# Kernel tuning notes

Measured on AMD Instinct MI355X. Metric: run time of the kernel, lower is better.

## Reference

```python
import jax, jax.numpy as jnp
import numpy as np

EMB_DIM = 32
UID_TGT = 200000
IID_TGT = 50000
BATCH = 128
TOPK = 50000          # hardcoded inside test_source_free branch
TARGET_LABEL = 4.0    # module-level target rating constant


def setup_inputs() -> dict:
    key = jax.random.key(0)
    k1, k2, k3, k4, k5 = jax.random.split(key, 5)
    # x: column 0 = item id (stored as float, like the torch code), cols 1: = src_rate_pre
    iid = jax.random.randint(k1, (BATCH,), 0, IID_TGT).astype(jnp.float32)
    src_rate = jax.random.normal(k2, (BATCH, EMB_DIM), dtype=jnp.float32)
    x = jnp.concatenate([iid[:, None], src_rate], axis=1)  # [B, 1+D]
    uid_weight = 0.1 * jax.random.normal(k3, (UID_TGT, EMB_DIM), dtype=jnp.float32)
    iid_weight = 0.1 * jax.random.normal(k4, (IID_TGT, EMB_DIM), dtype=jnp.float32)
    rp_weight = 0.1 * jax.random.normal(k5, (EMB_DIM, EMB_DIM), dtype=jnp.float32)
    return {"x": x, "uid_weight": uid_weight, "iid_weight": iid_weight, "rp_weight": rp_weight}


def reference(x, uid_weight, iid_weight, rp_weight):
    # === stage == 'test_source_free' ===
    iid = x[:, 0].astype(jnp.int32)                     # [B]
    iid_emb = iid_weight[iid]                           # [B, D] item embedding gather
    src_rate_pre = x[:, 1:] @ rp_weight.T               # [B, D] Linear(emb,emb,bias=False)
    # |uid_emb . src_rate - target|  (torch: [U,B]; here kept [B,U])
    predict_rate = jnp.abs(src_rate_pre @ uid_weight.T - TARGET_LABEL)  # [B, U]
    # torch: full sort ascending + take first TOPK  ==  bottom-TOPK per row
    _, topk_idx = jax.lax.top_k(-predict_rate, TOPK)    # [B, TOPK]
    # voted rating = <selected user emb, item emb>; compute all dots once,
    # then gather (same math as gathering [B,TOPK,D] embeddings and dotting).
    all_scores = iid_emb @ uid_weight.T                 # [B, U]
    voted_rating = jnp.take_along_axis(all_scores, topk_idx, axis=1)  # [B, TOPK]
    mean_rating = jnp.mean(voted_rating, axis=1)        # [B]
    return mean_rating
```

## Files before the change

### kernel.cpp

```cpp
#include <hip/hip_runtime.h>
#include <hip/hip_bf16.h>
#include <stdint.h>

#define EMB    32
#define BATCH  128
#define NU     200000
#define KSEL   50000
#define XCOLS  33
#define TILE   64
#define SLOTS  64

#define OFF_SPRE   0
#define OFF_IIDE   16384
#define OFF_GHIST  32768
#define OFF_BASE16 163840
#define OFF_PREFIX 164352
#define OFF_M2     164864
#define OFF_EQ     165376
#define OFF_CAND   173568

__global__ void prep_kernel(const float* __restrict__ x,
                            const float* __restrict__ iid_w,
                            const float* __restrict__ rp,
                            const float* __restrict__ uid,
                            float* __restrict__ s_pre,
                            float* __restrict__ iid_emb,
                            uint32_t* __restrict__ base16) {
    const int b = blockIdx.x;
    const int t = threadIdx.x;
    __shared__ float xr[EMB];
    if (t < EMB) xr[t] = x[b * XCOLS + 1 + t];
    __syncthreads();
    if (t < EMB) {
        float acc = 0.f;
        #pragma unroll
        for (int k = 0; k < EMB; ++k) acc += xr[k] * rp[t * EMB + k];
        s_pre[b * EMB + t] = acc;
    } else {
        const int d = t - EMB;
        const int iid = (int)x[b * XCOLS];
        iid_emb[b * EMB + d] = iid_w[(size_t)iid * EMB + d];
    }
    __syncthreads();
    if (t == 0) {
        float dot = 0.f;
        #pragma unroll
        for (int k = 0; k < EMB; ++k) dot += s_pre[b * EMB + k] * uid[k];
        const uint32_t bits = __float_as_uint(fabsf(dot - 4.0f));
        const uint32_t hi = bits >> 16;
        base16[b] = (hi > 128u) ? (hi - 128u) : 0u;
    }
}

__global__ void zero_kernel(uint32_t* __restrict__ p, int n) {
    int i = blockIdx.x * blockDim.x + threadIdx.x;
    if (i < n) p[i] = 0u;
}

__global__ __launch_bounds__(1024)
void sweep1_kernel(const float* __restrict__ s_pre,
                   const float* __restrict__ uid,
                   const uint32_t* __restrict__ base16,
                   uint32_t* __restrict__ ghist,
                   int jchunk) {
    extern __shared__ uint32_t smem1[];
    uint32_t* hist = smem1;
    float* tiles = (float*)(smem1 + 128 * 257);
    const int t  = threadIdx.x;
    const int b  = t & 127;
    const int jl = t >> 7;
    for (int i = t; i < 128 * 257; i += 1024) hist[i] = 0u;
    float s[EMB];
    #pragma unroll
    for (int d = 0; d < EMB; ++d) s[d] = s_pre[b * EMB + d];
    const uint32_t base = base16[b];

    const int j0 = blockIdx.x * jchunk;
    const int jend = min(j0 + jchunk, NU);
    const int nt = (jend - j0 + TILE - 1) / TILE;
    const int srow = t >> 4;
    const int sq   = t & 15;

    {
        const int j = j0 + srow;
        float2 v = make_float2(0.f, 0.f);
        if (j < NU) v = *(const float2*)(uid + (size_t)j * EMB + sq * 2);
        *(float2*)(tiles + srow * EMB + sq * 2) = v;
    }
    __syncthreads();

    for (int tt = 0; tt < nt; ++tt) {
        const int jt = j0 + tt * TILE;
        const bool has_next = (tt + 1 < nt);
        float2 vnext = make_float2(0.f, 0.f);
        if (has_next) {
            const int j = jt + TILE + srow;
            if (j < NU) vnext = *(const float2*)(uid + (size_t)j * EMB + sq * 2);
        }
        const float* tp = tiles + (tt & 1) * (TILE * EMB);
        const int lim = min(TILE, jend - jt);
        for (int jj = jl; jj < lim; jj += 8) {
            const float4* u4 = (const float4*)(tp + jj * EMB);
            float dot = 0.f;
            #pragma unroll
            for (int q = 0; q < 8; ++q) {
                float4 u = u4[q];
                dot += s[4*q+0]*u.x + s[4*q+1]*u.y + s[4*q+2]*u.z + s[4*q+3]*u.w;
            }
            const uint32_t bits = __float_as_uint(fabsf(dot - 4.0f));
            int digit = (int)(bits >> 16) - (int)base;
            digit = digit < 0 ? 0 : (digit > 255 ? 255 : digit);
            atomicAdd(&hist[b * 257 + digit], 1u);
        }
        if (has_next) {
            *(float2*)(tiles + ((tt + 1) & 1) * (TILE * EMB) + srow * EMB + sq * 2) = vnext;
        }
        __syncthreads();
    }
    for (int i = t; i < 128 * 256; i += 1024) {
        const uint32_t c = hist[(i >> 8) * 257 + (i & 255)];
        if (c) atomicAdd(&ghist[i], c);
    }
}

__global__ void scan1_kernel(const uint32_t* __restrict__ ghist,
                             const uint32_t* __restrict__ base16,
                             uint32_t* __restrict__ prefix16,
                             uint32_t* __restrict__ m2) {
    const int b = threadIdx.x;
    uint32_t cum = 0, before = 0;
    int c1 = 255;
    for (int d = 0; d < 256; ++d) {
        const uint32_t c = ghist[b * 256 + d];
        if (cum + c >= (uint32_t)KSEL) { c1 = d; before = cum; break; }
        cum += c;
        if (d == 255) before = cum;
    }
    prefix16[b] = base16[b] + (uint32_t)c1;
    m2[b] = (uint32_t)KSEL - before;
}

__global__ __launch_bounds__(1024)
void sweep2_kernel(const float* __restrict__ s_pre,
                   const float* __restrict__ iid_emb,
                   const float* __restrict__ uid,
                   const uint32_t* __restrict__ prefix16,
                   uint32_t* __restrict__ eq_cnt,
                   float* __restrict__ sum_part,
                   uint64_t* __restrict__ cand,
                   int cap, int jchunk) {
    extern __shared__ char smem2[];
    uint64_t* lcand = (uint64_t*)smem2;
    float*    tiles = (float*)(smem2 + 65536);
    uint32_t* lcnt  = (uint32_t*)(smem2 + 65536 + 16384);
    uint32_t* lbase = (uint32_t*)(smem2 + 65536 + 16384 + 512);
    float*    sums  = (float*)(smem2 + 65536 + 16384 + 1024);
    const int t  = threadIdx.x;
    const int b  = t & 127;
    const int jl = t >> 7;
    if (t < 128) lcnt[t] = 0u;
    float s[EMB], e[EMB];
    #pragma unroll
    for (int d = 0; d < EMB; ++d) { s[d] = s_pre[b*EMB+d]; e[d] = iid_emb[b*EMB+d]; }
    const uint32_t pfx = prefix16[b];

    const int j0 = blockIdx.x * jchunk;
    const int jend = min(j0 + jchunk, NU);
    const int nt = (jend - j0 + TILE - 1) / TILE;
    const int srow = t >> 4;
    const int sq   = t & 15;

    {
        const int j = j0 + srow;
        float2 v = make_float2(0.f, 0.f);
        if (j < NU) v = *(const float2*)(uid + (size_t)j * EMB + sq * 2);
        *(float2*)(tiles + srow * EMB + sq * 2) = v;
    }
    __syncthreads();

    float local = 0.f;
    for (int tt = 0; tt < nt; ++tt) {
        const int jt = j0 + tt * TILE;
        const bool has_next = (tt + 1 < nt);
        float2 vnext = make_float2(0.f, 0.f);
        if (has_next) {
            const int j = jt + TILE + srow;
            if (j < NU) vnext = *(const float2*)(uid + (size_t)j * EMB + sq * 2);
        }
        const float* tp = tiles + (tt & 1) * (TILE * EMB);
        const int lim = min(TILE, jend - jt);
        for (int jj = jl; jj < lim; jj += 8) {
            const float4* u4 = (const float4*)(tp + jj * EMB);
            float dot = 0.f, dv = 0.f;
            #pragma unroll
            for (int q = 0; q < 8; ++q) {
                float4 u = u4[q];
                dot += s[4*q+0]*u.x + s[4*q+1]*u.y + s[4*q+2]*u.z + s[4*q+3]*u.w;
                dv  += e[4*q+0]*u.x + e[4*q+1]*u.y + e[4*q+2]*u.z + e[4*q+3]*u.w;
            }
            const uint32_t bits = __float_as_uint(fabsf(dot - 4.0f));
            const uint32_t hi = bits >> 16;
            if (hi < pfx) {
                local += dv;
            } else if (hi == pfx) {
                const uint32_t pos = atomicAdd(&lcnt[b], 1u);
                const uint64_t pk = ((uint64_t)bits << 32) | (uint32_t)(jt + jj);
                if (pos < (uint32_t)SLOTS) {
                    lcand[b * SLOTS + pos] = pk;
                } else {
                    const uint32_t g = atomicAdd(&eq_cnt[b * 16], 1u);
                    if (g < (uint32_t)cap) cand[(size_t)b * cap + g] = pk;
                }
            }
        }
        if (has_next) {
            *(float2*)(tiles + ((tt + 1) & 1) * (TILE * EMB) + srow * EMB + sq * 2) = vnext;
        }
        __syncthreads();
    }
    sums[t] = local;
    __syncthreads();
    if (t < 128) {
        float acc = 0.f;
        #pragma unroll
        for (int l = 0; l < 8; ++l) acc += sums[l * 128 + t];
        sum_part[blockIdx.x * 128 + t] = acc;
        const uint32_t n = min(lcnt[t], (uint32_t)SLOTS);
        lbase[t] = atomicAdd(&eq_cnt[t * 16], n);
    }
    __syncthreads();
    for (int i = t; i < 128 * SLOTS; i += 1024) {
        const int bb = i >> 6;
        const int sl = i & 63;
        if (sl < (int)min(lcnt[bb], (uint32_t)SLOTS)) {
            const uint32_t p = lbase[bb] + (uint32_t)sl;
            if (p < (uint32_t)cap) cand[(size_t)bb * cap + p] = lcand[i];
        }
    }
}

__global__ __launch_bounds__(256)
void final_kernel(const float* __restrict__ iid_emb,
                  const float* __restrict__ uid,
                  const uint32_t* __restrict__ m2_,
                  const uint32_t* __restrict__ eq_cnt,
                  const float* __restrict__ sum_part,
                  const uint64_t* __restrict__ cand,
                  int cap, float* __restrict__ out) {
    const int b = blockIdx.x;
    const int t = threadIdx.x;
    __shared__ float red[256];
    __shared__ uint32_t hist[256];
    __shared__ float e[EMB];
    __shared__ uint32_t tie[128];
    __shared__ uint32_t tiecnt, sc2, sm3, sc3, sm4;
    __shared__ float sbelow;
    if (t < EMB) e[t] = iid_emb[b * EMB + t];
    if (t == 0) tiecnt = 0u;
    hist[t] = 0u;
    red[t] = sum_part[t * 128 + b];
    __syncthreads();
    for (int s = 128; s > 0; s >>= 1) { if (t < s) red[t] += red[t + s]; __syncthreads(); }
    if (t == 0) sbelow = red[0];
    __syncthreads();

    const uint32_t ec = eq_cnt[b * 16];
    const int cnt = (int)(ec < (uint32_t)cap ? ec : (uint32_t)cap);
    const uint64_t* cb = cand + (size_t)b * cap;

    for (int i = t; i < cnt; i += 256) {
        const uint32_t low16 = (uint32_t)(cb[i] >> 32) & 0xFFFFu;
        atomicAdd(&hist[low16 >> 8], 1u);
    }
    __syncthreads();
    if (t == 0) {
        const uint32_t m2v = m2_[b];
        uint32_t cum = 0, before = 0; int c2 = 255;
        for (int d = 0; d < 256; ++d) {
            const uint32_t c = hist[d];
            if (cum + c >= m2v) { c2 = d; before = cum; break; }
            cum += c;
        }
        sc2 = (uint32_t)c2; sm3 = m2v - before;
    }
    __syncthreads();
    const uint32_t c2 = sc2;
    hist[t] = 0u;
    __syncthreads();

    for (int i = t; i < cnt; i += 256) {
        const uint32_t low16 = (uint32_t)(cb[i] >> 32) & 0xFFFFu;
        if ((low16 >> 8) == c2) atomicAdd(&hist[low16 & 255u], 1u);
    }
    __syncthreads();
    if (t == 0) {
        const uint32_t m3 = sm3;
        uint32_t cum = 0, before = 0; int c3 = 255;
        for (int d = 0; d < 256; ++d) {
            const uint32_t c = hist[d];
            if (cum + c >= m3) { c3 = d; before = cum; break; }
            cum += c;
        }
        sc3 = (uint32_t)c3; sm4 = m3 - before;
    }
    __syncthreads();
    const uint32_t T16 = (c2 << 8) | sc3;

    float local = 0.f;
    for (int i = t; i < cnt; i += 256) {
        const uint64_t cv = cb[i];
        const uint32_t low16 = (uint32_t)(cv >> 32) & 0xFFFFu;
        if (low16 < T16) {
            const uint32_t j = (uint32_t)cv;
            const float4* u4 = (const float4*)(uid + (size_t)j * EMB);
            float dv = 0.f;
            #pragma unroll
            for (int q = 0; q < 8; ++q) {
                float4 u = u4[q];
                dv += e[4*q+0]*u.x + e[4*q+1]*u.y + e[4*q+2]*u.z + e[4*q+3]*u.w;
            }
            local += dv;
        } else if (low16 == T16) {
            const uint32_t pos = atomicAdd(&tiecnt, 1u);
            if (pos < 128u) tie[pos] = (uint32_t)cv;
        }
    }
    red[t] = local;
    __syncthreads();
    for (int s = 128; s > 0; s >>= 1) { if (t < s) red[t] += red[t + s]; __syncthreads(); }
    if (t == 0) {
        int tc = (int)(tiecnt < 128u ? tiecnt : 128u);
        for (int i = 1; i < tc; ++i) {
            const uint32_t v = tie[i]; int k = i - 1;
            while (k >= 0 && tie[k] > v) { tie[k+1] = tie[k]; --k; }
            tie[k+1] = v;
        }
        const int m4 = (int)sm4;
        float tsum = 0.f;
        for (int i = 0; i < m4 && i < tc; ++i) {
            const uint32_t j = tie[i];
            float dv = 0.f;
            for (int d = 0; d < EMB; ++d) dv += e[d] * uid[(size_t)j * EMB + d];
            tsum += dv;
        }
        out[b] = (sbelow + red[0] + tsum) / (float)KSEL;
    }
}

extern "C" void kernel_launch(void* const* d_in, const int* in_sizes, int n_in,
                              void* d_out, int out_size, void* d_ws, size_t ws_size,
                              hipStream_t stream) {
    const float* x     = (const float*)d_in[0];
    const float* uid   = (const float*)d_in[1];
    const float* iid_w = (const float*)d_in[2];
    const float* rp    = (const float*)d_in[3];
    float* out = (float*)d_out;

    char* ws = (char*)d_ws;
    float*    s_pre    = (float*)(ws + OFF_SPRE);
    float*    iid_emb  = (float*)(ws + OFF_IIDE);
    uint32_t* ghist    = (uint32_t*)(ws + OFF_GHIST);
    float*    sum_part = (float*)(ws + OFF_GHIST);
    uint32_t* base16   = (uint32_t*)(ws + OFF_BASE16);
    uint32_t* prefix16 = (uint32_t*)(ws + OFF_PREFIX);
    uint32_t* m2       = (uint32_t*)(ws + OFF_M2);
    uint32_t* eq_cnt   = (uint32_t*)(ws + OFF_EQ);
    uint64_t* cand     = (uint64_t*)(ws + OFF_CAND);

    long long cap_ll = ((long long)ws_size - OFF_CAND) / (128LL * 8LL);
    int cap = (int)(cap_ll > 16384 ? 16384 : (cap_ll < 1 ? 1 : cap_ll));

    {
        const int n = (OFF_CAND - OFF_GHIST) / 4;
        zero_kernel<<<(n + 255) / 256, 256, 0, stream>>>((uint32_t*)(ws + OFF_GHIST), n);
    }
    prep_kernel<<<BATCH, 64, 0, stream>>>(x, iid_w, rp, uid, s_pre, iid_emb, base16);

    const int JC = 782;
    const int G  = 256;
    sweep1_kernel<<<G, 1024, 128*257*4 + 2*TILE*EMB*4, stream>>>(s_pre, uid, base16, ghist, JC);

    scan1_kernel<<<1, 128, 0, stream>>>(ghist, base16, prefix16, m2);

    sweep2_kernel<<<G, 1024, 65536 + 16384 + 1024 + 4096, stream>>>(s_pre, iid_emb, uid,
                                                                    prefix16, eq_cnt, sum_part,
                                                                    cand, cap, JC);

    final_kernel<<<BATCH, 256, 0, stream>>>(iid_emb, uid, m2, eq_cnt, sum_part,
                                            cand, cap, out);
}
```

Baseline: 257.6 us.

## Replace LDS-tiled uid staging with wave-uniform scalar loads in both sweeps

Both sweep kernels stop staging uid rows through double-buffered shared-memory tiles. Instead, each wave reads its row index with readfirstlane and loads the row directly from global memory, so the loads can become scalar (broadcast) loads. Each thread also processes two rows per iteration to add ILP. This removes the LDS traffic and the per-tile barriers, and lowers shared-memory use, which may allow more resident blocks. The cost is reliance on the scalar cache and scalar load latency with no software prefetch.

After: 210.9 us. -18.1%, faster.

```diff
diff --git a/kernel.cpp b/kernel.cpp
--- a/kernel.cpp
+++ b/kernel.cpp
@@ -7,7 +7,6 @@
 #define NU     200000
 #define KSEL   50000
 #define XCOLS  33
-#define TILE   64
 #define SLOTS  64
 
 #define OFF_SPRE   0
@@ -63,9 +62,7 @@
                    const uint32_t* __restrict__ base16,
                    uint32_t* __restrict__ ghist,
                    int jchunk) {
-    extern __shared__ uint32_t smem1[];
-    uint32_t* hist = smem1;
-    float* tiles = (float*)(smem1 + 128 * 257);
+    extern __shared__ uint32_t hist[];
     const int t  = threadIdx.x;
     const int b  = t & 127;
     const int jl = t >> 7;
@@ -74,49 +71,39 @@
     #pragma unroll
     for (int d = 0; d < EMB; ++d) s[d] = s_pre[b * EMB + d];
     const uint32_t base = base16[b];
+    __syncthreads();
 
     const int j0 = blockIdx.x * jchunk;
     const int jend = min(j0 + jchunk, NU);
-    const int nt = (jend - j0 + TILE - 1) / TILE;
-    const int srow = t >> 4;
-    const int sq   = t & 15;
-
-    {
-        const int j = j0 + srow;
-        float2 v = make_float2(0.f, 0.f);
-        if (j < NU) v = *(const float2*)(uid + (size_t)j * EMB + sq * 2);
-        *(float2*)(tiles + srow * EMB + sq * 2) = v;
-    }
-    __syncthreads();
-
-    for (int tt = 0; tt < nt; ++tt) {
-        const int jt = j0 + tt * TILE;
-        const bool has_next = (tt + 1 < nt);
-        float2 vnext = make_float2(0.f, 0.f);
-        if (has_next) {
-            const int j = jt + TILE + srow;
-            if (j < NU) vnext = *(const float2*)(uid + (size_t)j * EMB + sq * 2);
-        }
-        const float* tp = tiles + (tt & 1) * (TILE * EMB);
-        const int lim = min(TILE, jend - jt);
-        for (int jj = jl; jj < lim; jj += 8) {
-            const float4* u4 = (const float4*)(tp + jj * EMB);
-            float dot = 0.f;
-            #pragma unroll
-            for (int q = 0; q < 8; ++q) {
-                float4 u = u4[q];
-                dot += s[4*q+0]*u.x + s[4*q+1]*u.y + s[4*q+2]*u.z + s[4*q+3]*u.w;
-            }
-            const uint32_t bits = __float_as_uint(fabsf(dot - 4.0f));
-            int digit = (int)(bits >> 16) - (int)base;
-            digit = digit < 0 ? 0 : (digit > 255 ? 255 : digit);
-            atomicAdd(&hist[b * 257 + digit], 1u);
-        }
-        if (has_next) {
-            *(float2*)(tiles + ((tt + 1) & 1) * (TILE * EMB) + srow * EMB + sq * 2) = vnext;
-        }
-        __syncthreads();
-    }
+    int j = j0 + jl;
+    for (; j + 8 < jend; j += 16) {
+        const int ju = __builtin_amdgcn_readfirstlane(j);
+        const float* up0 = uid + (size_t)ju * EMB;
+        const float* up1 = up0 + 8 * EMB;
+        float d0 = 0.f, d1 = 0.f;
+        #pragma unroll
+        for (int k = 0; k < EMB; ++k) {
+            d0 += s[k] * up0[k];
+            d1 += s[k] * up1[k];
+        }
+        const uint32_t bits0 = __float_as_uint(fabsf(d0 - 4.0f));
+        const uint32_t bits1 = __float_as_uint(fabsf(d1 - 4.0f));
+        int dg0 = (int)(bits0 >> 16) - (int)base; dg0 = dg0 < 0 ? 0 : (dg0 > 255 ? 255 : dg0);
+        int dg1 = (int)(bits1 >> 16) - (int)base; dg1 = dg1 < 0 ? 0 : (dg1 > 255 ? 255 : dg1);
+        atomicAdd(&hist[b * 257 + dg0], 1u);
+        atomicAdd(&hist[b * 257 + dg1], 1u);
+    }
+    for (; j < jend; j += 8) {
+        const int ju = __builtin_amdgcn_readfirstlane(j);
+        const float* up0 = uid + (size_t)ju * EMB;
+        float d0 = 0.f;
+        #pragma unroll
+        for (int k = 0; k < EMB; ++k) d0 += s[k] * up0[k];
+        const uint32_t bits0 = __float_as_uint(fabsf(d0 - 4.0f));
+        int dg0 = (int)(bits0 >> 16) - (int)base; dg0 = dg0 < 0 ? 0 : (dg0 > 255 ? 255 : dg0);
+        atomicAdd(&hist[b * 257 + dg0], 1u);
+    }
+    __syncthreads();
     for (int i = t; i < 128 * 256; i += 1024) {
         const uint32_t c = hist[(i >> 8) * 257 + (i & 255)];
         if (c) atomicAdd(&ghist[i], c);
@@ -151,10 +138,9 @@
                    int cap, int jchunk) {
     extern __shared__ char smem2[];
     uint64_t* lcand = (uint64_t*)smem2;
-    float*    tiles = (float*)(smem2 + 65536);
-    uint32_t* lcnt  = (uint32_t*)(smem2 + 65536 + 16384);
-    uint32_t* lbase = (uint32_t*)(smem2 + 65536 + 16384 + 512);
-    float*    sums  = (float*)(smem2 + 65536 + 16384 + 1024);
+    uint32_t* lcnt  = (uint32_t*)(smem2 + 65536);
+    uint32_t* lbase = (uint32_t*)(smem2 + 66048);
+    float*    sums  = (float*)(smem2 + 66560);
     const int t  = threadIdx.x;
     const int b  = t & 127;
     const int jl = t >> 7;
@@ -163,60 +149,68 @@
     #pragma unroll
     for (int d = 0; d < EMB; ++d) { s[d] = s_pre[b*EMB+d]; e[d] = iid_emb[b*EMB+d]; }
     const uint32_t pfx = prefix16[b];
+    __syncthreads();
 
     const int j0 = blockIdx.x * jchunk;
     const int jend = min(j0 + jchunk, NU);
-    const int nt = (jend - j0 + TILE - 1) / TILE;
-    const int srow = t >> 4;
-    const int sq   = t & 15;
-
-    {
-        const int j = j0 + srow;
-        float2 v = make_float2(0.f, 0.f);
-        if (j < NU) v = *(const float2*)(uid + (size_t)j * EMB + sq * 2);
-        *(float2*)(tiles + srow * EMB + sq * 2) = v;
-    }
-    __syncthreads();
-
     float local = 0.f;
-    for (int tt = 0; tt < nt; ++tt) {
-        const int jt = j0 + tt * TILE;
-        const bool has_next = (tt + 1 < nt);
-        float2 vnext = make_float2(0.f, 0.f);
-        if (has_next) {
-            const int j = jt + TILE + srow;
-            if (j < NU) vnext = *(const float2*)(uid + (size_t)j * EMB + sq * 2);
-        }
-        const float* tp = tiles + (tt & 1) * (TILE * EMB);
-        const int lim = min(TILE, jend - jt);
-        for (int jj = jl; jj < lim; jj += 8) {
-            const float4* u4 = (const float4*)(tp + jj * EMB);
-            float dot = 0.f, dv = 0.f;
-            #pragma unroll
-            for (int q = 0; q < 8; ++q) {
-                float4 u = u4[q];
-                dot += s[4*q+0]*u.x + s[4*q+1]*u.y + s[4*q+2]*u.z + s[4*q+3]*u.w;
-                dv  += e[4*q+0]*u.x + e[4*q+1]*u.y + e[4*q+2]*u.z + e[4*q+3]*u.w;
+    int j = j0 + jl;
+    for (; j + 8 < jend; j += 16) {
+        const int ju = __builtin_amdgcn_readfirstlane(j);
+        const float* up0 = uid + (size_t)ju * EMB;
+        const float* up1 = up0 + 8 * EMB;
+        float d0 = 0.f, v0 = 0.f, d1 = 0.f, v1 = 0.f;
+        #pragma unroll
+        for (int k = 0; k < EMB; ++k) {
+            const float u0 = up0[k], u1 = up1[k];
+            d0 += s[k] * u0;  v0 += e[k] * u0;
+            d1 += s[k] * u1;  v1 += e[k] * u1;
+        }
+        const uint32_t bits0 = __float_as_uint(fabsf(d0 - 4.0f));
+        const uint32_t bits1 = __float_as_uint(fabsf(d1 - 4.0f));
+        const uint32_t hi0 = bits0 >> 16, hi1 = bits1 >> 16;
+        if (hi0 < pfx) local += v0;
+        else if (hi0 == pfx) {
+            const uint32_t pos = atomicAdd(&lcnt[b], 1u);
+            const uint64_t pk = ((uint64_t)bits0 << 32) | (uint32_t)j;
+            if (pos < (uint32_t)SLOTS) lcand[b * SLOTS + pos] = pk;
+            else {
+                const uint32_t g = atomicAdd(&eq_cnt[b * 16], 1u);
+                if (g < (uint32_t)cap) cand[(size_t)b * cap + g] = pk;
             }
-            const uint32_t bits = __float_as_uint(fabsf(dot - 4.0f));
-            const uint32_t hi = bits >> 16;
-            if (hi < pfx) {
-                local += dv;
-            } else if (hi == pfx) {
-                const uint32_t pos = atomicAdd(&lcnt[b], 1u);
-                const uint64_t pk = ((uint64_t)bits << 32) | (uint32_t)(jt + jj);
-                if (pos < (uint32_t)SLOTS) {
-                    lcand[b * SLOTS + pos] = pk;
-                } else {
-                    const uint32_t g = atomicAdd(&eq_cnt[b * 16], 1u);
-                    if (g < (uint32_t)cap) cand[(size_t)b * cap + g] = pk;
-                }
+        }
+        if (hi1 < pfx) local += v1;
+        else if (hi1 == pfx) {
+            const uint32_t pos = atomicAdd(&lcnt[b], 1u);
+            const uint64_t pk = ((uint64_t)bits1 << 32) | (uint32_t)(j + 8);
+            if (pos < (uint32_t)SLOTS) lcand[b * SLOTS + pos] = pk;
+            else {
+                const uint32_t g = atomicAdd(&eq_cnt[b * 16], 1u);
+                if (g < (uint32_t)cap) cand[(size_t)b * cap + g] = pk;
             }
         }
-        if (has_next) {
-            *(float2*)(tiles + ((tt + 1) & 1) * (TILE * EMB) + srow * EMB + sq * 2) = vnext;
-        }
-        __syncthreads();
+    }
+    for (; j < jend; j += 8) {
+        const int ju = __builtin_amdgcn_readfirstlane(j);
+        const float* up0 = uid + (size_t)ju * EMB;
+        float d0 = 0.f, v0 = 0.f;
+        #pragma unroll
+        for (int k = 0; k < EMB; ++k) {
+            const float u0 = up0[k];
+            d0 += s[k] * u0;  v0 += e[k] * u0;
+        }
+        const uint32_t bits0 = __float_as_uint(fabsf(d0 - 4.0f));
+        const uint32_t hi0 = bits0 >> 16;
+        if (hi0 < pfx) local += v0;
+        else if (hi0 == pfx) {
+            const uint32_t pos = atomicAdd(&lcnt[b], 1u);
+            const uint64_t pk = ((uint64_t)bits0 << 32) | (uint32_t)j;
+            if (pos < (uint32_t)SLOTS) lcand[b * SLOTS + pos] = pk;
+            else {
+                const uint32_t g = atomicAdd(&eq_cnt[b * 16], 1u);
+                if (g < (uint32_t)cap) cand[(size_t)b * cap + g] = pk;
+            }
+        }
     }
     sums[t] = local;
     __syncthreads();
@@ -378,13 +372,13 @@
 
     const int JC = 782;
     const int G  = 256;
-    sweep1_kernel<<<G, 1024, 128*257*4 + 2*TILE*EMB*4, stream>>>(s_pre, uid, base16, ghist, JC);
+    sweep1_kernel<<<G, 1024, 128 * 257 * 4, stream>>>(s_pre, uid, base16, ghist, JC);
 
     scan1_kernel<<<1, 128, 0, stream>>>(ghist, base16, prefix16, m2);
 
-    sweep2_kernel<<<G, 1024, 65536 + 16384 + 1024 + 4096, stream>>>(s_pre, iid_emb, uid,
-                                                                    prefix16, eq_cnt, sum_part,
-                                                                    cand, cap, JC);
+    sweep2_kernel<<<G, 1024, 65536 + 512 + 512 + 4096, stream>>>(s_pre, iid_emb, uid,
+                                                                 prefix16, eq_cnt, sum_part,
+                                                                 cand, cap, JC);
 
     final_kernel<<<BATCH, 256, 0, stream>>>(iid_emb, uid, m2, eq_cnt, sum_part,
                                             cand, cap, out);
```
